# Optimization experiments

Measured on AMD Instinct MI355X. Metric: run time of the kernel, lower is better.

The kernel has to match this reference:

```python
import jax, jax.numpy as jnp
import numpy as np

N = 100000  # nodes

def gcn_layer(x, W, b, src, dst, norm):
    # x: [N, Fin] -> [N, Fout]; symmetric-normalized aggregation (PyG GCNConv)
    h = x @ W                                   # linear first (no bias yet)
    msg = h[src] * norm[:, None]                # gather + edge-wise scale
    out = jax.ops.segment_sum(msg, dst, num_segments=N)  # scatter-add to targets
    return out + b

def _prep_edges(edge_index):
    # add self loops
    loops = jnp.arange(N, dtype=edge_index.dtype)
    src = jnp.concatenate([edge_index[0], loops])
    dst = jnp.concatenate([edge_index[1], loops])
    # deg computed on target nodes with unit edge weights
    deg = jax.ops.segment_sum(jnp.ones_like(dst, dtype=jnp.float32), dst, num_segments=N)
    dinv = jnp.where(deg > 0, jax.lax.rsqrt(deg), 0.0)
    norm = dinv[src] * dinv[dst]
    return src, dst, norm

def setup_inputs() -> dict:
    key = jax.random.key(0)
    ks = jax.random.split(key, 8)
    F_in, H1, H2, C = 512, 256, 64, 10
    E = 3200000
    x = jax.random.normal(ks[0], (N, F_in), dtype=jnp.float32)
    edge_index = jax.random.randint(ks[1], (2, E), 0, N, dtype=jnp.int64)
    def glorot(k, fan_in, fan_out):
        s = jnp.sqrt(6.0 / (fan_in + fan_out))
        return jax.random.uniform(k, (fan_in, fan_out), jnp.float32, -s, s)
    return {
        "x": x,
        "edge_index": edge_index,
        "W1": glorot(ks[2], F_in, H1), "b1": jnp.zeros((H1,), jnp.float32),
        "W2": glorot(ks[3], H1, H2),   "b2": jnp.zeros((H2,), jnp.float32),
        "W3": glorot(ks[4], H2, C),    "b3": jnp.zeros((C,), jnp.float32),
    }

def reference(x, edge_index, W1, b1, W2, b2, W3, b3):
    src, dst, norm = _prep_edges(edge_index)
    h = jax.nn.relu(gcn_layer(x, W1, b1, src, dst, norm))
    h = jax.nn.relu(gcn_layer(h, W2, b2, src, dst, norm))
    h = gcn_layer(h, W3, b3, src, dst, norm)
    return jax.nn.log_softmax(h, axis=1)
```

## Files before the change

### kernel.cpp

```cpp
#include <hip/hip_runtime.h>
#include <math.h>

#define NNODES 100000
#define NEDGES 3200000
#define NB 391
#define PB 512
#define CHUNK 6250

typedef __attribute__((ext_vector_type(4))) float f32x4;
typedef __attribute__((ext_vector_type(2))) float f32x2;
typedef __attribute__((ext_vector_type(8))) short bf16x8;

__device__ __forceinline__ float bf2f(ushort u) {
    union { unsigned u; float f; } v; v.u = ((unsigned)u) << 16; return v.f;
}
__device__ __forceinline__ ushort f2bf(float f) {
    union { float f; unsigned u; } v; v.f = f;
    unsigned r = v.u + 0x7FFFu + ((v.u >> 16) & 1u);
    return (ushort)(r >> 16);
}

__device__ __forceinline__ unsigned pack_bf2(float f0, float f1) {
    union { float f; unsigned u; } a, b; a.f = f0; b.f = f1;
#if __has_builtin(__builtin_amdgcn_perm)
    return __builtin_amdgcn_perm(b.u, a.u, 0x07060302u);
#else
    return (b.u & 0xFFFF0000u) | (a.u >> 16);
#endif
}

#if __has_builtin(__builtin_amdgcn_cvt_pk_fp8_f32) && __has_builtin(__builtin_amdgcn_cvt_pk_f32_fp8)
#define FP8_HW 1
#else
#define FP8_HW 0
#endif

__device__ __forceinline__ unsigned fp8enc_sw(float f) {
    union { float f; unsigned u; } v; v.f = f;
    unsigned sign = v.u >> 31;
    float a = fabsf(f);
    if (a >= 448.0f) return (sign << 7) | 0x7E;
    if (a < 0.0009765625f) return sign << 7;
    unsigned u = v.u & 0x7FFFFFFFu;
    u += 0x7FFFFu + ((u >> 20) & 1u);
    int e2 = (int)(u >> 23) - 127;
    if (e2 < -6) {
        int m = (int)(a * 512.0f + 0.5f); if (m > 7) m = 7;
        return (sign << 7) | (unsigned)m;
    }
    if (e2 > 8) return (sign << 7) | 0x7E;
    unsigned mant = (u >> 20) & 7u;
    return (sign << 7) | ((unsigned)(e2 + 7) << 3) | mant;
}
__device__ __forceinline__ float fp8dec_sw(unsigned b) {
    unsigned s = b >> 7, e = (b >> 3) & 0xF, m = b & 7;
    float v;
    if (e == 0) v = (float)m * 0.001953125f;
    else { union { unsigned u; float f; } x; x.u = ((e + 120u) << 23) | (m << 20); v = x.f; }
    return s ? -v : v;
}

__device__ __forceinline__ unsigned char f2fp8(float f) {
#if FP8_HW
    return (unsigned char)(__builtin_amdgcn_cvt_pk_fp8_f32(f, 0.f, 0, false) & 0xFF);
#else
    return (unsigned char)fp8enc_sw(f);
#endif
}
__device__ __forceinline__ void fp8x4_acc2(unsigned w, f32x2& a01, f32x2& a23) {
#if FP8_HW
    a01 += __builtin_amdgcn_cvt_pk_f32_fp8((int)w, false);
    a23 += __builtin_amdgcn_cvt_pk_f32_fp8((int)w, true);
#else
    a01[0] += fp8dec_sw(w & 0xFF); a01[1] += fp8dec_sw((w >> 8) & 0xFF);
    a23[0] += fp8dec_sw((w >> 16) & 0xFF); a23[1] += fp8dec_sw(w >> 24);
#endif
}

__global__ void bucket_hist(const int* __restrict__ dst, int e, int* __restrict__ hist,
                            const float* __restrict__ W1, ushort* __restrict__ W1t,
                            const float* __restrict__ W2, unsigned char* __restrict__ W2t,
                            const float* __restrict__ W3, unsigned char* __restrict__ W3t) {
    __shared__ int h[NB];
    const int b = blockIdx.x, t = threadIdx.x;
    for (int j = t; j < NB; j += 256) h[j] = 0;
    __syncthreads();
    const int lo = b * CHUNK;
    int hi = lo + CHUNK; if (hi > e) hi = e;
    for (int i = lo + t; i < hi; i += 256)
        atomicAdd(&h[dst[i] >> 8], 1);
    {
        const int stride = PB * 256;
        for (int idx = b * 256 + t; idx < 256 * 512 + 64 * 256 + 16 * 64; idx += stride) {
            if (idx < 256 * 512) {
                int nn = idx / 512, k = idx % 512;
                W1t[idx] = f2bf(W1[(size_t)k * 256 + nn]);
            } else if (idx < 256 * 512 + 64 * 256) {
                int r = idx - 256 * 512;
                int nn = r / 256, k = r % 256;
                W2t[r] = f2fp8(W2[(size_t)k * 64 + nn]);
            } else {
                int r = idx - 256 * 512 - 64 * 256;
                int nn = r / 64, k = r % 64;
                W3t[r] = (nn < 10) ? f2fp8(W3[(size_t)k * 10 + nn]) : (unsigned char)0;
            }
        }
    }
    __syncthreads();
    for (int j = t; j < NB; j += 256) hist[b * NB + j] = h[j];
}

__global__ void scan_buckets(int* __restrict__ hist, int* __restrict__ btotal) {
    __shared__ int s[256];
    const int j = blockIdx.x, t = threadIdx.x;
    int v0 = hist[(2 * t) * NB + j];
    int v1 = hist[(2 * t + 1) * NB + j];
    int p = v0 + v1;
    s[t] = p;
    __syncthreads();
    for (int off = 1; off < 256; off <<= 1) {
        int u = (t >= off) ? s[t - off] : 0;
        __syncthreads();
        s[t] += u;
        __syncthreads();
    }
    int excl = s[t] - p;
    hist[(2 * t) * NB + j] = excl;
    hist[(2 * t + 1) * NB + j] = excl + v0;
    if (t == 255) btotal[j] = s[255];
}

__global__ void scan_btotal(const int* __restrict__ btotal, int* __restrict__ bstart, int e) {
    __shared__ int s[512];
    const int t = threadIdx.x;
    int v = (t < NB) ? btotal[t] : 0;
    s[t] = v;
    __syncthreads();
    for (int off = 1; off < 512; off <<= 1) {
        int u = (t >= off) ? s[t - off] : 0;
        __syncthreads();
        s[t] += u;
        __syncthreads();
    }
    if (t < NB) bstart[t] = s[t] - v;
    if (t == 0) bstart[NB] = e;
}

__global__ void bucket_scatter(const int* __restrict__ src, const int* __restrict__ dst, int e,
                               const int* __restrict__ hist, const int* __restrict__ bstart,
                               unsigned* __restrict__ bucketed) {
    __shared__ int off[NB];
    const int b = blockIdx.x, t = threadIdx.x;
    for (int j = t; j < NB; j += 256) off[j] = bstart[j] + hist[b * NB + j];
    __syncthreads();
    const int lo = b * CHUNK;
    int hi = lo + CHUNK; if (hi > e) hi = e;
    for (int i = lo + t; i < hi; i += 256) {
        int d = dst[i];
        int j = d >> 8;
        int p = atomicAdd(&off[j], 1);
        bucketed[p] = (unsigned)src[i] | ((unsigned)(d & 255) << 24);
    }
}

__global__ void bucket_finalize(const unsigned* __restrict__ bucketed, const int* __restrict__ bstart,
                                float* __restrict__ dinv, int* __restrict__ rowptr,
                                int* __restrict__ esrc, int n, int e) {
    __shared__ int h[256];
    __shared__ int s[256];
    __shared__ int rp[256];
    const int j = blockIdx.x, t = threadIdx.x;
    h[t] = 0;
    __syncthreads();
    const int lo = bstart[j], hi = bstart[j + 1];
    for (int i = lo + t; i < hi; i += 256)
        atomicAdd(&h[bucketed[i] >> 24], 1);
    __syncthreads();
    const int c = h[t] + 1;
    s[t] = c;
    __syncthreads();
    for (int off = 1; off < 256; off <<= 1) {
        int u = (t >= off) ? s[t - off] : 0;
        __syncthreads();
        s[t] += u;
        __syncthreads();
    }
    const int excl = s[t] - c;
    const int base = j << 8;
    const int node = base + t;
    const int myrp = bstart[j] + base + excl;
    rp[t] = myrp;
    if (node < n) {
        dinv[node] = rsqrtf((float)c);
        rowptr[node] = myrp;
        esrc[myrp] = node;
    }
    if (j == 0 && t == 0) rowptr[n] = e + n;
    h[t] = 0;
    __syncthreads();
    for (int i = lo + t; i < hi; i += 256) {
        unsigned ed = bucketed[i];
        int l = ed >> 24;
        int off = atomicAdd(&h[l], 1);
        esrc[rp[l] + 1 + off] = (int)(ed & 0xFFFFFFu);
    }
}

template <int BM, int BN, int BK, int WM, int WN>
__launch_bounds__(WM* WN * 64)
__global__ void gemm_f32a(const float* __restrict__ A, const ushort* __restrict__ Bt,
                          const float* __restrict__ dinv, unsigned char* __restrict__ Cout,
                          int M, int N, int K) {
    constexpr int NT = WM * WN * 64;
    __shared__ __align__(16) float Asf[BM][BK];
    __shared__ __align__(16) ushort Bs[BN][BK];
    const int tid = threadIdx.x;
    const int wid = tid >> 6, lane = tid & 63;
    const int wr = wid / WN, wc = wid % WN;
    constexpr int TM = BM / WM, TN = BN / WN;
    constexpr int FM = TM / 16, FN = TN / 16;
    const int m0 = blockIdx.y * BM, n0 = blockIdx.x * BN;
    const int ln = lane & 15, ks4 = (lane >> 4) * 2;

    f32x4 acc[FM][FN] = {};

    constexpr int CPRA = BK / 4;
    constexpr int ACH = BM * CPRA;
    constexpr int CPRB = BK / 8;
    constexpr int BCH = BN * CPRB;

    for (int k0 = 0; k0 < K; k0 += BK) {
        #pragma unroll
        for (int it = 0; it < ACH / NT; ++it) {
            int c = it * NT + tid;
            int row = c >> 3, chs = c & 7;
            int gch = chs ^ (row & 7);
            int gm = m0 + row; if (gm >= M) gm = M - 1;
            const float* gp = &A[(size_t)gm * K + k0 + gch * 4];
            __builtin_amdgcn_global_load_lds(
                (const __attribute__((address_space(1))) void*)gp,
                (__attribute__((address_space(3))) void*)((char*)&Asf[0][0] + c * 16),
                16, 0, 0);
        }
        #pragma unroll
        for (int it = 0; it < BCH / NT; ++it) {
            int c = it * NT + tid;
            int row = c / CPRB, ch = c % CPRB;
            const ushort* gp = &Bt[(size_t)(n0 + row) * K + k0 + ch * 8];
            __builtin_amdgcn_global_load_lds(
                (const __attribute__((address_space(1))) void*)gp,
                (__attribute__((address_space(3))) void*)((char*)&Bs[0][0] + c * 16),
                16, 0, 0);
        }
        __syncthreads();

        bf16x8 af[FM], bfr[FN];
        #pragma unroll
        for (int mi = 0; mi < FM; ++mi) {
            int r = wr * TM + mi * 16 + ln;
            const char* rowp = (const char*)&Asf[0][0] + r * (BK * 4);
            float4 a0 = *(const float4*)(rowp + ((ks4 ^ (r & 7)) * 16));
            float4 a1 = *(const float4*)(rowp + (((ks4 + 1) ^ (r & 7)) * 16));
            union { unsigned w[4]; bf16x8 v; } u;
            u.w[0] = pack_bf2(a0.x, a0.y);
            u.w[1] = pack_bf2(a0.z, a0.w);
            u.w[2] = pack_bf2(a1.x, a1.y);
            u.w[3] = pack_bf2(a1.z, a1.w);
            af[mi] = u.v;
        }
        const int ks = (lane >> 4) * 8;
        #pragma unroll
        for (int nj = 0; nj < FN; ++nj)
            bfr[nj] = *(const bf16x8*)&Bs[wc * TN + nj * 16 + ln][ks];
        #pragma unroll
        for (int mi = 0; mi < FM; ++mi)
            #pragma unroll
            for (int nj = 0; nj < FN; ++nj)
                acc[mi][nj] = __builtin_amdgcn_mfma_f32_16x16x32_bf16(af[mi], bfr[nj], acc[mi][nj], 0, 0, 0);
        __syncthreads();
    }

    const int rbase = (lane >> 4) * 4;
    #pragma unroll
    for (int mi = 0; mi < FM; ++mi) {
        #pragma unroll
        for (int r = 0; r < 4; ++r) {
            int gm = m0 + wr * TM + mi * 16 + rbase + r;
            if (gm >= M) continue;
            float d = dinv[gm];
            #pragma unroll
            for (int nj = 0; nj < FN; ++nj) {
                int gn = n0 + wc * TN + nj * 16 + ln;
                Cout[(size_t)gm * N + gn] = f2fp8(acc[mi][nj][r] * d);
            }
        }
    }
}

template <int BM, int BN, int BK, int WM, int WN, int OUTK>
__launch_bounds__(WM* WN * 64)
__global__ void gemm_fp8(const unsigned char* __restrict__ A, const unsigned char* __restrict__ Bt,
                         const float* __restrict__ dinv, void* __restrict__ Cout,
                         int M, int N, int K) {
    constexpr int NT = WM * WN * 64;
    __shared__ __align__(16) unsigned char As[BM][BK];
    __shared__ __align__(16) unsigned char Bs[BN][BK];
    const int tid = threadIdx.x;
    const int wid = tid >> 6, lane = tid & 63;
    const int wr = wid / WN, wc = wid % WN;
    constexpr int TM = BM / WM, TN = BN / WN;
    constexpr int FM = TM / 16, FN = TN / 16;
    const int m0 = blockIdx.y * BM, n0 = blockIdx.x * BN;
    const int ln = lane & 15;

    f32x4 acc[FM][FN] = {};

    constexpr int CPR = BK / 16;
    constexpr int ACH = BM * CPR;
    constexpr int BCH = BN * CPR;

    for (int k0 = 0; k0 < K; k0 += BK) {
        #pragma unroll
        for (int it = 0; it < (ACH + NT - 1) / NT; ++it) {
            int c = it * NT + tid;
            if ((ACH % NT == 0) || (c < ACH)) {
                int row = c / CPR, ch = c % CPR;
                int gm = m0 + row; if (gm >= M) gm = M - 1;
                const unsigned char* gp = &A[(size_t)gm * K + k0 + ch * 16];
                __builtin_amdgcn_global_load_lds(
                    (const __attribute__((address_space(1))) void*)gp,
                    (__attribute__((address_space(3))) void*)((char*)&As[0][0] + c * 16),
                    16, 0, 0);
            }
        }
        #pragma unroll
        for (int it = 0; it < (BCH + NT - 1) / NT; ++it) {
            int c = it * NT + tid;
            if ((BCH % NT == 0) || (c < BCH)) {
                int row = c / CPR, ch = c % CPR;
                const unsigned char* gp = &Bt[(size_t)(n0 + row) * K + k0 + ch * 16];
                __builtin_amdgcn_global_load_lds(
                    (const __attribute__((address_space(1))) void*)gp,
                    (__attribute__((address_space(3))) void*)((char*)&Bs[0][0] + c * 16),
                    16, 0, 0);
            }
        }
        __syncthreads();

        long af[FM], bfr[FN];
        #pragma unroll
        for (int mi = 0; mi < FM; ++mi)
            af[mi] = ((const long*)&As[0][0])[(wr * TM + mi * 16 + ln) * (BK / 8) + (lane >> 4)];
        #pragma unroll
        for (int nj = 0; nj < FN; ++nj)
            bfr[nj] = ((const long*)&Bs[0][0])[(wc * TN + nj * 16 + ln) * (BK / 8) + (lane >> 4)];
        #pragma unroll
        for (int mi = 0; mi < FM; ++mi)
            #pragma unroll
            for (int nj = 0; nj < FN; ++nj)
                acc[mi][nj] = __builtin_amdgcn_mfma_f32_16x16x32_fp8_fp8(af[mi], bfr[nj], acc[mi][nj], 0, 0, 0);
        __syncthreads();
    }

    const int rbase = (lane >> 4) * 4;
    #pragma unroll
    for (int mi = 0; mi < FM; ++mi) {
        #pragma unroll
        for (int r = 0; r < 4; ++r) {
            int gm = m0 + wr * TM + mi * 16 + rbase + r;
            if (gm >= M) continue;
            float d = dinv[gm];
            #pragma unroll
            for (int nj = 0; nj < FN; ++nj) {
                int gn = n0 + wc * TN + nj * 16 + ln;
                float v = acc[mi][nj][r] * d;
                if (OUTK == 0) ((ushort*)Cout)[(size_t)gm * N + gn] = f2bf(v);
                else           ((unsigned char*)Cout)[(size_t)gm * N + gn] = f2fp8(v);
            }
        }
    }
}

__global__ void agg1_fp8(const unsigned* __restrict__ h, const int* __restrict__ rowptr,
                         const int* __restrict__ esrc, const float* __restrict__ dinv,
                         const float* __restrict__ bias, unsigned char* __restrict__ out, int n) {
    const int wid = threadIdx.x >> 6, lane = threadIdx.x & 63;
    const int i = blockIdx.x * 4 + wid;
    if (i >= n) return;
    const int lo = rowptr[i], hi = rowptr[i + 1];
    f32x2 a01 = {0.f, 0.f}, a23 = {0.f, 0.f};
    int e = lo;
    for (; e + 7 < hi; e += 8) {
        int s[8];
        unsigned w[8];
        #pragma unroll
        for (int q = 0; q < 8; ++q) s[q] = esrc[e + q];
        #pragma unroll
        for (int q = 0; q < 8; ++q) w[q] = h[(size_t)s[q] * 64 + lane];
        #pragma unroll
        for (int q = 0; q < 8; ++q) fp8x4_acc2(w[q], a01, a23);
    }
    for (; e < hi; ++e)
        fp8x4_acc2(h[(size_t)esrc[e] * 64 + lane], a01, a23);

    float d = dinv[i];
    const int f0 = lane * 4;
    float4 b = *(const float4*)&bias[f0];
    uchar4 o;
    o.x = f2fp8(fmaxf(a01[0] * d + b.x, 0.f));
    o.y = f2fp8(fmaxf(a01[1] * d + b.y, 0.f));
    o.z = f2fp8(fmaxf(a23[0] * d + b.z, 0.f));
    o.w = f2fp8(fmaxf(a23[1] * d + b.w, 0.f));
    *(uchar4*)&out[(size_t)i * 256 + f0] = o;
}

__global__ void agg2_fp8(const unsigned* __restrict__ h, const int* __restrict__ rowptr,
                         const int* __restrict__ esrc, const float* __restrict__ dinv,
                         const float* __restrict__ bias, unsigned char* __restrict__ out, int n) {
    const int g = threadIdx.x >> 4, j = threadIdx.x & 15;
    const int i = blockIdx.x * 16 + g;
    if (i >= n) return;
    const int lo = rowptr[i], hi = rowptr[i + 1];
    f32x2 a01 = {0.f, 0.f}, a23 = {0.f, 0.f};
    int e = lo;
    for (; e + 7 < hi; e += 8) {
        int s[8];
        unsigned w[8];
        #pragma unroll
        for (int q = 0; q < 8; ++q) s[q] = esrc[e + q];
        #pragma unroll
        for (int q = 0; q < 8; ++q) w[q] = h[(size_t)s[q] * 16 + j];
        #pragma unroll
        for (int q = 0; q < 8; ++q) fp8x4_acc2(w[q], a01, a23);
    }
    for (; e < hi; ++e)
        fp8x4_acc2(h[(size_t)esrc[e] * 16 + j], a01, a23);

    float d = dinv[i];
    const int f0 = j * 4;
    float4 b = *(const float4*)&bias[f0];
    uchar4 o;
    o.x = f2fp8(fmaxf(a01[0] * d + b.x, 0.f));
    o.y = f2fp8(fmaxf(a01[1] * d + b.y, 0.f));
    o.z = f2fp8(fmaxf(a23[0] * d + b.z, 0.f));
    o.w = f2fp8(fmaxf(a23[1] * d + b.w, 0.f));
    *(uchar4*)&out[(size_t)i * 64 + f0] = o;
}

__global__ void agg3_logsoftmax(const ushort* __restrict__ h3, const int* __restrict__ rowptr,
                                const int* __restrict__ esrc, const float* __restrict__ dinv,
                                const float* __restrict__ bias, float* __restrict__ out, int n) {
    const int g = threadIdx.x >> 3, j = threadIdx.x & 7;
    const int i = blockIdx.x * 32 + g;
    if (i >= n) return;
    const int lo = rowptr[i], hi = rowptr[i + 1];
    float a0 = 0.f, a1 = 0.f;
    int e = lo;
    for (; e + 3 < hi; e += 4) {
        int s0 = esrc[e], s1 = esrc[e + 1], s2 = esrc[e + 2], s3 = esrc[e + 3];
        unsigned w0 = *(const unsigned*)&h3[(size_t)s0 * 16 + 2 * j];
        unsigned w1 = *(const unsigned*)&h3[(size_t)s1 * 16 + 2 * j];
        unsigned w2 = *(const unsigned*)&h3[(size_t)s2 * 16 + 2 * j];
        unsigned w3 = *(const unsigned*)&h3[(size_t)s3 * 16 + 2 * j];
        a0 += bf2f((ushort)(w0 & 0xFFFF)) + bf2f((ushort)(w1 & 0xFFFF))
            + bf2f((ushort)(w2 & 0xFFFF)) + bf2f((ushort)(w3 & 0xFFFF));
        a1 += bf2f((ushort)(w0 >> 16)) + bf2f((ushort)(w1 >> 16))
            + bf2f((ushort)(w2 >> 16)) + bf2f((ushort)(w3 >> 16));
    }
    for (; e < hi; ++e) {
        unsigned w = *(const unsigned*)&h3[(size_t)esrc[e] * 16 + 2 * j];
        a0 += bf2f((ushort)(w & 0xFFFF));
        a1 += bf2f((ushort)(w >> 16));
    }
    const int f0 = 2 * j;
    float d = dinv[i];
    float v0 = (f0 < 10) ? (a0 * d + bias[f0]) : -INFINITY;
    float v1 = (f0 + 1 < 10) ? (a1 * d + bias[f0 + 1]) : -INFINITY;
    float m = fmaxf(v0, v1);
    #pragma unroll
    for (int off = 1; off < 8; off <<= 1) m = fmaxf(m, __shfl_xor(m, off, 8));
    float ex = ((f0 < 10) ? expf(v0 - m) : 0.f) + ((f0 + 1 < 10) ? expf(v1 - m) : 0.f);
    #pragma unroll
    for (int off = 1; off < 8; off <<= 1) ex += __shfl_xor(ex, off, 8);
    float ls = logf(ex);
    if (f0 < 10)     out[(size_t)i * 10 + f0] = v0 - m - ls;
    if (f0 + 1 < 10) out[(size_t)i * 10 + f0 + 1] = v1 - m - ls;
}

extern "C" void kernel_launch(void* const* d_in, const int* in_sizes, int n_in,
                              void* d_out, int out_size, void* d_ws, size_t ws_size,
                              hipStream_t stream) {
    const int N = NNODES, E = NEDGES;
    const float* x  = (const float*)d_in[0];
    const int*   ei = (const int*)d_in[1];
    const float* W1 = (const float*)d_in[2];
    const float* b1 = (const float*)d_in[3];
    const float* W2 = (const float*)d_in[4];
    const float* b2 = (const float*)d_in[5];
    const float* W3 = (const float*)d_in[6];
    const float* b3 = (const float*)d_in[7];
    float* out = (float*)d_out;
    const int* src = ei;
    const int* dst = ei + E;

    char* ws = (char*)d_ws;
    size_t off = 0;
    auto alloc = [&](size_t bytes) -> void* {
        void* p = ws + off;
        off = (off + bytes + 255) & ~(size_t)255;
        return p;
    };
    float* dinv   = (float*)alloc((size_t)N * 4);
    int*   rowptr = (int*)alloc((size_t)(N + 1) * 4);
    int*   btotal = (int*)alloc((size_t)NB * 4);
    int*   bstart = (int*)alloc((size_t)(NB + 1) * 4);
    int*   esrc   = (int*)alloc((size_t)(E + N) * 4);
    ushort* W1t   = (ushort*)alloc((size_t)256 * 512 * 2);
    unsigned char* W2t8 = (unsigned char*)alloc((size_t)64 * 256);
    unsigned char* W3t8 = (unsigned char*)alloc((size_t)16 * 64);
    ushort* h3b   = (ushort*)alloc((size_t)N * 16 * 2);
    ushort* buf1  = (ushort*)alloc((size_t)N * 256 * 2);
    ushort* buf2  = (ushort*)alloc((size_t)N * 256 * 2);
    int*   hist   = (int*)buf1;
    unsigned* bucketed = (unsigned*)buf2;
    unsigned char* h1fp8 = (unsigned char*)buf1;
    unsigned char* a1fp8 = (unsigned char*)buf2;
    unsigned char* h2fp8 = (unsigned char*)buf1;
    unsigned char* a2fp8 = (unsigned char*)buf2;

    const int T = 256;
    bucket_hist<<<PB, T, 0, stream>>>(dst, E, hist, W1, W1t, W2, W2t8, W3, W3t8);
    scan_buckets<<<NB, T, 0, stream>>>(hist, btotal);
    scan_btotal<<<1, 512, 0, stream>>>(btotal, bstart, E);
    bucket_scatter<<<PB, T, 0, stream>>>(src, dst, E, hist, bstart, bucketed);
    bucket_finalize<<<NB, T, 0, stream>>>(bucketed, bstart, dinv, rowptr, esrc, N, E);

    const int MB = (N + 127) / 128;

    gemm_f32a<128, 256, 32, 2, 4><<<dim3(1, MB), 512, 0, stream>>>(x, W1t, dinv, h1fp8, N, 256, 512);
    agg1_fp8<<<(N + 3) / 4, 256, 0, stream>>>((const unsigned*)h1fp8, rowptr, esrc, dinv, b1, a1fp8, N);

    gemm_fp8<128, 64, 32, 2, 2, 2><<<dim3(1, MB), 256, 0, stream>>>(a1fp8, W2t8, dinv, h2fp8, N, 64, 256);
    agg2_fp8<<<(N + 15) / 16, 256, 0, stream>>>((const unsigned*)h2fp8, rowptr, esrc, dinv, b2, a2fp8, N);

    gemm_fp8<128, 16, 32, 4, 1, 0><<<dim3(1, MB), 256, 0, stream>>>(a2fp8, W3t8, dinv, h3b, N, 16, 64);
    agg3_logsoftmax<<<(N + 31) / 32, 256, 0, stream>>>(h3b, rowptr, esrc, dinv, b3, out, N);
}
```

Baseline: 373.6 us.

## Cache bucket edges in LDS, deepen agg1 unroll, split agg2 features across blocks

bucket_finalize now keeps each bucket's edges in a shared-memory cache on the first pass, so the second pass reads them from LDS instead of global memory, falling back to global past the cache size. agg1 gathers 16 edges per iteration with a 4-edge tail loop to keep more loads in flight. agg2 splits the 64 features into two halves handled by different blocks, with 8 lanes per node and 32 nodes per block. Blocks are ordered so both halves of the same node range run close together, aiming for L2 reuse of the index arrays and smaller per-node transactions. The changes cost extra LDS (which may limit occupancy), more registers, and twice the edge-index reads in agg2.

After: 395.3 us. 1.06x slower.

```diff
diff --git a/kernel.cpp b/kernel.cpp
--- a/kernel.cpp
+++ b/kernel.cpp
@@ -6,6 +6,7 @@
 #define NB 391
 #define PB 512
 #define CHUNK 6250
+#define ECAP 9216
 
 typedef __attribute__((ext_vector_type(4))) float f32x4;
 typedef __attribute__((ext_vector_type(2))) float f32x2;
@@ -169,12 +170,18 @@
     __shared__ int h[256];
     __shared__ int s[256];
     __shared__ int rp[256];
+    __shared__ unsigned ecache[ECAP];
     const int j = blockIdx.x, t = threadIdx.x;
     h[t] = 0;
     __syncthreads();
     const int lo = bstart[j], hi = bstart[j + 1];
-    for (int i = lo + t; i < hi; i += 256)
-        atomicAdd(&h[bucketed[i] >> 24], 1);
+    const int ecnt = hi - lo;
+    for (int i = lo + t; i < hi; i += 256) {
+        unsigned ed = bucketed[i];
+        int idx = i - lo;
+        if (idx < ECAP) ecache[idx] = ed;
+        atomicAdd(&h[ed >> 24], 1);
+    }
     __syncthreads();
     const int c = h[t] + 1;
     s[t] = c;
@@ -198,8 +205,8 @@
     if (j == 0 && t == 0) rowptr[n] = e + n;
     h[t] = 0;
     __syncthreads();
-    for (int i = lo + t; i < hi; i += 256) {
-        unsigned ed = bucketed[i];
+    for (int idx = t; idx < ecnt; idx += 256) {
+        unsigned ed = (idx < ECAP) ? ecache[idx] : bucketed[lo + idx];
         int l = ed >> 24;
         int off = atomicAdd(&h[l], 1);
         esrc[rp[l] + 1 + off] = (int)(ed & 0xFFFFFFu);
@@ -390,15 +397,25 @@
     const int lo = rowptr[i], hi = rowptr[i + 1];
     f32x2 a01 = {0.f, 0.f}, a23 = {0.f, 0.f};
     int e = lo;
-    for (; e + 7 < hi; e += 8) {
-        int s[8];
-        unsigned w[8];
-        #pragma unroll
-        for (int q = 0; q < 8; ++q) s[q] = esrc[e + q];
-        #pragma unroll
-        for (int q = 0; q < 8; ++q) w[q] = h[(size_t)s[q] * 64 + lane];
-        #pragma unroll
-        for (int q = 0; q < 8; ++q) fp8x4_acc2(w[q], a01, a23);
+    for (; e + 15 < hi; e += 16) {
+        int s[16];
+        unsigned w[16];
+        #pragma unroll
+        for (int q = 0; q < 16; ++q) s[q] = esrc[e + q];
+        #pragma unroll
+        for (int q = 0; q < 16; ++q) w[q] = h[(size_t)s[q] * 64 + lane];
+        #pragma unroll
+        for (int q = 0; q < 16; ++q) fp8x4_acc2(w[q], a01, a23);
+    }
+    for (; e + 3 < hi; e += 4) {
+        int s[4];
+        unsigned w[4];
+        #pragma unroll
+        for (int q = 0; q < 4; ++q) s[q] = esrc[e + q];
+        #pragma unroll
+        for (int q = 0; q < 4; ++q) w[q] = h[(size_t)s[q] * 64 + lane];
+        #pragma unroll
+        for (int q = 0; q < 4; ++q) fp8x4_acc2(w[q], a01, a23);
     }
     for (; e < hi; ++e)
         fp8x4_acc2(h[(size_t)esrc[e] * 64 + lane], a01, a23);
@@ -417,10 +434,15 @@
 __global__ void agg2_fp8(const unsigned* __restrict__ h, const int* __restrict__ rowptr,
                          const int* __restrict__ esrc, const float* __restrict__ dinv,
                          const float* __restrict__ bias, unsigned char* __restrict__ out, int n) {
-    const int g = threadIdx.x >> 4, j = threadIdx.x & 15;
-    const int i = blockIdx.x * 16 + g;
+    const int bid = blockIdx.x;
+    const int g8 = bid & 7;
+    const int half = g8 >> 2;
+    const int seq = (bid >> 3) * 4 + (g8 & 3);
+    const int g = threadIdx.x >> 3, j = threadIdx.x & 7;
+    const int i = seq * 32 + g;
     if (i >= n) return;
     const int lo = rowptr[i], hi = rowptr[i + 1];
+    const unsigned* hh = h + half * 8 + j;
     f32x2 a01 = {0.f, 0.f}, a23 = {0.f, 0.f};
     int e = lo;
     for (; e + 7 < hi; e += 8) {
@@ -429,15 +451,15 @@
         #pragma unroll
         for (int q = 0; q < 8; ++q) s[q] = esrc[e + q];
         #pragma unroll
-        for (int q = 0; q < 8; ++q) w[q] = h[(size_t)s[q] * 16 + j];
+        for (int q = 0; q < 8; ++q) w[q] = hh[(size_t)s[q] * 16];
         #pragma unroll
         for (int q = 0; q < 8; ++q) fp8x4_acc2(w[q], a01, a23);
     }
     for (; e < hi; ++e)
-        fp8x4_acc2(h[(size_t)esrc[e] * 16 + j], a01, a23);
+        fp8x4_acc2(hh[(size_t)esrc[e] * 16], a01, a23);
 
     float d = dinv[i];
-    const int f0 = j * 4;
+    const int f0 = half * 32 + j * 4;
     float4 b = *(const float4*)&bias[f0];
     uchar4 o;
     o.x = f2fp8(fmaxf(a01[0] * d + b.x, 0.f));
@@ -541,7 +563,11 @@
     agg1_fp8<<<(N + 3) / 4, 256, 0, stream>>>((const unsigned*)h1fp8, rowptr, esrc, dinv, b1, a1fp8, N);
 
     gemm_fp8<128, 64, 32, 2, 2, 2><<<dim3(1, MB), 256, 0, stream>>>(a1fp8, W2t8, dinv, h2fp8, N, 64, 256);
-    agg2_fp8<<<(N + 15) / 16, 256, 0, stream>>>((const unsigned*)h2fp8, rowptr, esrc, dinv, b2, a2fp8, N);
+    {
+        const int nseq = (N + 31) / 32;
+        const int g2 = 8 * ((nseq + 3) / 4);
+        agg2_fp8<<<g2, 256, 0, stream>>>((const unsigned*)h2fp8, rowptr, esrc, dinv, b2, a2fp8, N);
+    }
 
     gemm_fp8<128, 16, 32, 4, 1, 0><<<dim3(1, MB), 256, 0, stream>>>(a2fp8, W3t8, dinv, h3b, N, 16, 64);
     agg3_logsoftmax<<<(N + 31) / 32, 256, 0, stream>>>(h3b, rowptr, esrc, dinv, b3, out, N);
```
